# Kernel tuning notes

Hardware: AMD Instinct MI355X
Metric: run time of the kernel (lower is better)

Reference implementation:

```python
import jax, jax.numpy as jnp
from jax import lax
import numpy as np

K = 3          # sampling grid size (kernel_size)
WS = 4         # scope kernel size (weight_shape)
DILATION = 1


def setup_inputs() -> dict:
    key = jax.random.key(0)
    k1, k2, k3, k4 = jax.random.split(key, 4)
    x = jax.random.normal(k1, (4, 128, 56, 56), jnp.float32)
    # offset conv is zero-initialized in the original; use small values so offsets are realistic
    offset_w = jax.random.normal(k2, (2 * K * K, 128, K, K), jnp.float32) * 0.01
    offset_b = jax.random.normal(k3, (2 * K * K,), jnp.float32) * 0.01
    weight = jax.random.normal(k4, (128, WS, WS), jnp.float32) * 0.1  # depthwise scope kernel
    return {"x": x, "offset_w": offset_w, "offset_b": offset_b, "weight": weight}


def reference(x, offset_w, offset_b, weight):
    B, C, H, W = x.shape
    K2 = K * K
    # offset conv: 3x3, stride 1, pad 1 (same geometry as main conv)
    off = lax.conv_general_dilated(
        x, offset_w, window_strides=(1, 1), padding=[(1, 1), (1, 1)],
        dimension_numbers=("NCHW", "OIHW", "NCHW"))
    off = off + offset_b[None, :, None, None]
    off = off * DILATION                     # offset_clip is None
    off = off.reshape(B, K2, 2, H, W)
    dy, dx = off[:, :, 0], off[:, :, 1]      # [B,K2,H,W]

    # base coordinates of the KxK sampling grid centered inside the WSxWS scope kernel
    base = jnp.arange(K, dtype=x.dtype) - (K - 1) / 2 + (WS - 1) / 2   # [K]
    by = jnp.repeat(base, K)                 # k = i*K + j -> row i
    bx = jnp.tile(base, K)                   # k = i*K + j -> col j
    yc = dy + by[None, :, None, None]        # [B,K2,H,W] sampling coords in kernel space
    xc = dx + bx[None, :, None, None]

    # bilinear sampling of the scope kernel (zero outside scope)
    wflat = weight.reshape(C, WS * WS)
    y0 = jnp.floor(yc)
    x0 = jnp.floor(xc)
    samp = jnp.zeros((C, B, K2, H, W), x.dtype)
    for oy, ox in ((0, 0), (0, 1), (1, 0), (1, 1)):
        yi = y0 + oy
        xi = x0 + ox
        coef = (1.0 - jnp.abs(yc - yi)) * (1.0 - jnp.abs(xc - xi))
        valid = (yi >= 0) & (yi < WS) & (xi >= 0) & (xi < WS)
        idx = (jnp.clip(yi, 0, WS - 1) * WS + jnp.clip(xi, 0, WS - 1)).astype(jnp.int32)
        vals = jnp.take(wflat, idx, axis=1)  # [C,B,K2,H,W] irregular gather
        samp = samp + (coef * valid)[None] * vals
    samp = jnp.moveaxis(samp, 0, 1)          # [B,C,K2,H,W]

    # depthwise conv with per-pixel sampled kernels (stride 1, pad 1, dilation 1)
    xp = jnp.pad(x, ((0, 0), (0, 0), (1, 1), (1, 1)))
    pats = jnp.stack([xp[:, :, i:i + H, j:j + W] for i in range(K) for j in range(K)], axis=2)
    return jnp.sum(samp * pats, axis=2)      # [B,C,H,W]
```

## Files before the change

kernel.cpp:

```cpp
#include <hip/hip_runtime.h>

#define BB 4
#define CC 128
#define HH 56
#define WW 56
#define NK2 9
#define NO 18
#define WSZ 4
#define CG 8
#define CPG 16
#define W64 64

#define WSA_FLOATS (224L * CG * NO * W64)
#define WSC_ENTRIES (4L * NK2 * HH * W64)

__global__ __launch_bounds__(256) void conv_partial(
    const float* __restrict__ x,
    const float* __restrict__ offset_w,
    float* __restrict__ wsA)
{
    const int blk = blockIdx.x;
    const int bh  = blk >> 3;
    const int cg  = blk & 7;
    const int b   = bh / HH;
    const int h   = bh - b * HH;
    const int t   = threadIdx.x;
    const int lane = t & 63;
    const int wv  = __builtin_amdgcn_readfirstlane(t >> 6);

    __shared__ float s_red[4][NO][W64];

    float acc[NO];
    #pragma unroll
    for (int o = 0; o < NO; ++o) acc[o] = 0.f;

    const int c0 = cg * CPG + wv * 4;
    if (lane < WW) {
        const float* xb = x + (long)b * CC * HH * WW;
        #pragma unroll
        for (int ci = 0; ci < 4; ++ci) {
            const int c = c0 + ci;
            const float* xc = xb + c * HH * WW;
            #pragma unroll
            for (int ky = 0; ky < 3; ++ky) {
                const int hy = h + ky - 1;
                float x0 = 0.f, x1 = 0.f, x2 = 0.f;
                if (hy >= 0 && hy < HH) {
                    const float* r = xc + hy * WW;
                    x1 = r[lane];
                    x0 = (lane > 0)      ? r[lane - 1] : 0.f;
                    x2 = (lane < WW - 1) ? r[lane + 1] : 0.f;
                }
                const float* wp = offset_w + c * 9 + ky * 3;
                #pragma unroll
                for (int o = 0; o < NO; ++o) {
                    const float* wo = wp + o * (CC * 9);
                    acc[o] += x0 * wo[0] + x1 * wo[1] + x2 * wo[2];
                }
            }
        }
    }
    #pragma unroll
    for (int o = 0; o < NO; ++o) s_red[wv][o][lane] = acc[o];
    __syncthreads();

    const float* sr = (const float*)s_red;
    float* dst = wsA + (long)blk * (NO * W64);
    for (int s = t; s < NO * W64; s += 256) {
        dst[s] = sr[s] + sr[NO * W64 + s] + sr[2 * NO * W64 + s] + sr[3 * NO * W64 + s];
    }
}

__global__ __launch_bounds__(64) void coef_kernel(
    const float* __restrict__ wsA,
    const float* __restrict__ offset_b,
    float4* __restrict__ wsC,
    unsigned* __restrict__ wsI)
{
    const int blk = blockIdx.x;
    const int k2  = blk % NK2;
    const int bh  = blk / NK2;
    const int b   = bh / HH;
    const int h   = bh - b * HH;
    const int w   = threadIdx.x;

    const float* base = wsA + (long)bh * (CG * NO * W64);
    float dy = offset_b[2 * k2];
    float dx = offset_b[2 * k2 + 1];
    #pragma unroll
    for (int g = 0; g < CG; ++g) {
        dy += base[g * (NO * W64) + (2 * k2) * W64 + w];
        dx += base[g * (NO * W64) + (2 * k2 + 1) * W64 + w];
    }

    const float yc = dy + 0.5f + (float)(k2 / 3);
    const float xc = dx + 0.5f + (float)(k2 % 3);
    const float y0 = floorf(yc), x0f = floorf(xc);
    const float fy = yc - y0, fx = xc - x0f;
    const int yi = (int)y0, xi = (int)x0f;
    float cf[4]; int id[4];
    #pragma unroll
    for (int q = 0; q < 4; ++q) {
        const int oy = q >> 1, ox = q & 1;
        const int yy = yi + oy, xx = xi + ox;
        float c2 = (oy ? fy : 1.f - fy) * (ox ? fx : 1.f - fx);
        const bool valid = (yy >= 0) && (yy < WSZ) && (xx >= 0) && (xx < WSZ);
        cf[q] = valid ? c2 : 0.f;
        const int yyc = yy < 0 ? 0 : (yy > 3 ? 3 : yy);
        const int xxc = xx < 0 ? 0 : (xx > 3 ? 3 : xx);
        id[q] = yyc * 4 + xxc;
    }
    const long oidx = ((long)(b * NK2 + k2) * HH + h) * W64 + w;
    wsC[oidx] = make_float4(cf[0], cf[1], cf[2], cf[3]);
    wsI[oidx] = (unsigned)(id[0] | (id[1] << 4) | (id[2] << 8) | (id[3] << 12));
}

__global__ __launch_bounds__(256) void sample_kernel(
    const float* __restrict__ x,
    const float* __restrict__ weight,
    const float4* __restrict__ wsC,
    const unsigned* __restrict__ wsI,
    float* __restrict__ out)
{
    const int blk = blockIdx.x;
    const int bh  = blk >> 3;
    const int cg  = blk & 7;
    const int b   = bh / HH;
    const int h   = bh - b * HH;
    const int t   = threadIdx.x;
    const int lane = t & 63;
    const int wv  = __builtin_amdgcn_readfirstlane(t >> 6);

    __shared__ float s_w[CPG][16];
    if (t < CPG * 16) ((float*)s_w)[t] = weight[cg * CPG * 16 + t];
    __syncthreads();

    if (lane >= WW) return;
    const int w = lane;

    float4 cf[NK2]; unsigned pk[NK2];
    const long cidx0 = ((long)b * NK2 * HH + h) * W64 + w;
    #pragma unroll
    for (int k2 = 0; k2 < NK2; ++k2) {
        cf[k2] = wsC[cidx0 + (long)k2 * HH * W64];
        pk[k2] = wsI[cidx0 + (long)k2 * HH * W64];
    }

    const int cl0 = wv * 4;
    #pragma unroll
    for (int u = 0; u < 4; ++u) {
        const int cl = cl0 + u;
        const int c  = cg * CPG + cl;
        const float* xc = x + ((long)b * CC + c) * HH * WW;
        float xv[9];
        #pragma unroll
        for (int ky = 0; ky < 3; ++ky) {
            const int hy = h + ky - 1;
            #pragma unroll
            for (int kx = 0; kx < 3; ++kx) {
                const int wx = w + kx - 1;
                float v = 0.f;
                if (hy >= 0 && hy < HH && wx >= 0 && wx < WW)
                    v = xc[hy * WW + wx];
                xv[ky * 3 + kx] = v;
            }
        }
        float res = 0.f;
        #pragma unroll
        for (int k2 = 0; k2 < NK2; ++k2) {
            const unsigned p = pk[k2];
            const float samp = cf[k2].x * s_w[cl][p & 15]
                             + cf[k2].y * s_w[cl][(p >> 4) & 15]
                             + cf[k2].z * s_w[cl][(p >> 8) & 15]
                             + cf[k2].w * s_w[cl][(p >> 12) & 15];
            res += samp * xv[k2];
        }
        out[(((long)b * CC + c) * HH + h) * WW + w] = res;
    }
}

extern "C" void kernel_launch(void* const* d_in, const int* in_sizes, int n_in,
                              void* d_out, int out_size, void* d_ws, size_t ws_size,
                              hipStream_t stream) {
    const float* x        = (const float*)d_in[0];
    const float* offset_w = (const float*)d_in[1];
    const float* offset_b = (const float*)d_in[2];
    const float* weight   = (const float*)d_in[3];
    float* out = (float*)d_out;

    float*    wsA = (float*)d_ws;
    float4*   wsC = (float4*)((char*)d_ws + WSA_FLOATS * 4);
    unsigned* wsI = (unsigned*)((char*)d_ws + WSA_FLOATS * 4 + WSC_ENTRIES * 16);

    conv_partial <<<224 * CG, 256, 0, stream>>>(x, offset_w, wsA);
    coef_kernel  <<<224 * NK2, 64, 0, stream>>>(wsA, offset_b, wsC, wsI);
    sample_kernel<<<224 * CG, 256, 0, stream>>>(x, weight, wsC, wsI, out);
}
```

Measured before the change: 110.5 us.

## Compute two output rows per block in offset conv and stage weights in LDS

The offset-conv kernel now handles two output rows per block. It loads four input rows once and reuses each weight for both rows. Its weights are staged in shared memory and read as float4, replacing scattered global loads. The sampling kernel stores the scope weights transposed, so one float4 LDS read serves four channels at once. The cost is more registers and fewer blocks in the conv kernel, which may lower occupancy.

```diff
diff --git a/kernel.cpp b/kernel.cpp
--- a/kernel.cpp
+++ b/kernel.cpp
@@ -20,54 +20,85 @@
     float* __restrict__ wsA)
 {
     const int blk = blockIdx.x;
-    const int bh  = blk >> 3;
+    const int bh2 = blk >> 3;
     const int cg  = blk & 7;
-    const int b   = bh / HH;
-    const int h   = bh - b * HH;
+    const int b   = bh2 / 28;
+    const int h2  = bh2 - b * 28;
+    const int h0  = 2 * h2;
     const int t   = threadIdx.x;
     const int lane = t & 63;
     const int wv  = __builtin_amdgcn_readfirstlane(t >> 6);
 
-    __shared__ float s_red[4][NO][W64];
-
-    float acc[NO];
-    #pragma unroll
-    for (int o = 0; o < NO; ++o) acc[o] = 0.f;
-
-    const int c0 = cg * CPG + wv * 4;
+    __shared__ float s_wt[CPG][3][56];
+    __shared__ float s_red[4][2][NO][W64];
+
+    for (int i = t; i < CPG * 3 * 54; i += 256) {
+        const int ci = i / 162;
+        int r = i - ci * 162;
+        const int ky = r / 54;
+        r -= ky * 54;
+        const int o = r / 3, kx = r - o * 3;
+        s_wt[ci][ky][r] = offset_w[(o * CC + cg * CPG + ci) * 9 + ky * 3 + kx];
+    }
+    __syncthreads();
+
+    float acc[2][NO];
+    #pragma unroll
+    for (int r = 0; r < 2; ++r)
+        #pragma unroll
+        for (int o = 0; o < NO; ++o) acc[r][o] = 0.f;
+
     if (lane < WW) {
         const float* xb = x + (long)b * CC * HH * WW;
         #pragma unroll
         for (int ci = 0; ci < 4; ++ci) {
-            const int c = c0 + ci;
+            const int cl = wv * 4 + ci;
+            const int c  = cg * CPG + cl;
             const float* xc = xb + c * HH * WW;
+            float xr[4][3];
+            #pragma unroll
+            for (int r = 0; r < 4; ++r) {
+                const int hy = h0 + r - 1;
+                float v0 = 0.f, v1 = 0.f, v2 = 0.f;
+                if (hy >= 0 && hy < HH) {
+                    const float* row = xc + hy * WW;
+                    v1 = row[lane];
+                    v0 = (lane > 0)      ? row[lane - 1] : 0.f;
+                    v2 = (lane < WW - 1) ? row[lane + 1] : 0.f;
+                }
+                xr[r][0] = v0; xr[r][1] = v1; xr[r][2] = v2;
+            }
             #pragma unroll
             for (int ky = 0; ky < 3; ++ky) {
-                const int hy = h + ky - 1;
-                float x0 = 0.f, x1 = 0.f, x2 = 0.f;
-                if (hy >= 0 && hy < HH) {
-                    const float* r = xc + hy * WW;
-                    x1 = r[lane];
-                    x0 = (lane > 0)      ? r[lane - 1] : 0.f;
-                    x2 = (lane < WW - 1) ? r[lane + 1] : 0.f;
-                }
-                const float* wp = offset_w + c * 9 + ky * 3;
+                const float4* wq = (const float4*)&s_wt[cl][ky][0];
+                float4 w4[14];
                 #pragma unroll
-                for (int o = 0; o < NO; ++o) {
-                    const float* wo = wp + o * (CC * 9);
-                    acc[o] += x0 * wo[0] + x1 * wo[1] + x2 * wo[2];
+                for (int q = 0; q < 14; ++q) w4[q] = wq[q];
+                #pragma unroll
+                for (int f = 0; f < 54; ++f) {
+                    const int o = f / 3, kx = f - o * 3;
+                    const int q = f >> 2, e = f & 3;
+                    const float wv_ = (e == 0) ? w4[q].x : (e == 1) ? w4[q].y
+                                     : (e == 2) ? w4[q].z : w4[q].w;
+                    acc[0][o] += wv_ * xr[ky][kx];
+                    acc[1][o] += wv_ * xr[ky + 1][kx];
                 }
             }
         }
     }
     #pragma unroll
-    for (int o = 0; o < NO; ++o) s_red[wv][o][lane] = acc[o];
+    for (int r = 0; r < 2; ++r)
+        #pragma unroll
+        for (int o = 0; o < NO; ++o) s_red[wv][r][o][lane] = acc[r][o];
     __syncthreads();
 
     const float* sr = (const float*)s_red;
-    float* dst = wsA + (long)blk * (NO * W64);
-    for (int s = t; s < NO * W64; s += 256) {
-        dst[s] = sr[s] + sr[NO * W64 + s] + sr[2 * NO * W64 + s] + sr[3 * NO * W64 + s];
+    for (int s = t; s < 2 * NO * W64; s += 256) {
+        const float v = sr[s] + sr[2304 + s] + sr[2 * 2304 + s] + sr[3 * 2304 + s];
+        const int r = s / (NO * W64);
+        const int rem = s - r * (NO * W64);
+        const int bh = b * HH + h0 + r;
+        wsA[((long)bh * CG + cg) * (NO * W64) + rem] = v;
     }
 }
 
@@ -131,12 +162,16 @@
     const int lane = t & 63;
     const int wv  = __builtin_amdgcn_readfirstlane(t >> 6);
 
-    __shared__ float s_w[CPG][16];
-    if (t < CPG * 16) ((float*)s_w)[t] = weight[cg * CPG * 16 + t];
+    __shared__ float s_wT[16][20];
+    if (t < 256) {
+        const int j = t >> 4, cl = t & 15;
+        s_wT[j][cl] = weight[(cg * CPG + cl) * 16 + j];
+    }
     __syncthreads();
 
     if (lane >= WW) return;
     const int w = lane;
+    const int cl0 = wv * 4;
 
     float4 cf[NK2]; unsigned pk[NK2];
     const long cidx0 = ((long)b * NK2 * HH + h) * W64 + w;
@@ -146,13 +181,11 @@
         pk[k2] = wsI[cidx0 + (long)k2 * HH * W64];
     }
 
-    const int cl0 = wv * 4;
+    float xv[4][9];
     #pragma unroll
     for (int u = 0; u < 4; ++u) {
-        const int cl = cl0 + u;
-        const int c  = cg * CPG + cl;
+        const int c = cg * CPG + cl0 + u;
         const float* xc = x + ((long)b * CC + c) * HH * WW;
-        float xv[9];
         #pragma unroll
         for (int ky = 0; ky < 3; ++ky) {
             const int hy = h + ky - 1;
@@ -162,20 +195,33 @@
                 float v = 0.f;
                 if (hy >= 0 && hy < HH && wx >= 0 && wx < WW)
                     v = xc[hy * WW + wx];
-                xv[ky * 3 + kx] = v;
+                xv[u][ky * 3 + kx] = v;
             }
         }
-        float res = 0.f;
-        #pragma unroll
-        for (int k2 = 0; k2 < NK2; ++k2) {
-            const unsigned p = pk[k2];
-            const float samp = cf[k2].x * s_w[cl][p & 15]
-                             + cf[k2].y * s_w[cl][(p >> 4) & 15]
-                             + cf[k2].z * s_w[cl][(p >> 8) & 15]
-                             + cf[k2].w * s_w[cl][(p >> 12) & 15];
-            res += samp * xv[k2];
-        }
-        out[(((long)b * CC + c) * HH + h) * WW + w] = res;
+    }
+
+    float res[4] = {0.f, 0.f, 0.f, 0.f};
+    #pragma unroll
+    for (int k2 = 0; k2 < NK2; ++k2) {
+        const unsigned p = pk[k2];
+        const float4 W0 = *(const float4*)&s_wT[p & 15][cl0];
+        const float4 W1 = *(const float4*)&s_wT[(p >> 4) & 15][cl0];
+        const float4 W2 = *(const float4*)&s_wT[(p >> 8) & 15][cl0];
+        const float4 W3 = *(const float4*)&s_wT[(p >> 12) & 15][cl0];
+        const float4 c4 = cf[k2];
+        float samp[4];
+        samp[0] = c4.x * W0.x + c4.y * W1.x + c4.z * W2.x + c4.w * W3.x;
+        samp[1] = c4.x * W0.y + c4.y * W1.y + c4.z * W2.y + c4.w * W3.y;
+        samp[2] = c4.x * W0.z + c4.y * W1.z + c4.z * W2.z + c4.w * W3.z;
+        samp[3] = c4.x * W0.w + c4.y * W1.w + c4.z * W2.w + c4.w * W3.w;
+        #pragma unroll
+        for (int u = 0; u < 4; ++u) res[u] += samp[u] * xv[u][k2];
+    }
+
+    #pragma unroll
+    for (int u = 0; u < 4; ++u) {
+        const int c = cg * CPG + cl0 + u;
+        out[(((long)b * CC + c) * HH + h) * WW + w] = res[u];
     }
 }
 
@@ -192,7 +238,7 @@
     float4*   wsC = (float4*)((char*)d_ws + WSA_FLOATS * 4);
     unsigned* wsI = (unsigned*)((char*)d_ws + WSA_FLOATS * 4 + WSC_ENTRIES * 16);
 
-    conv_partial <<<224 * CG, 256, 0, stream>>>(x, offset_w, wsA);
+    conv_partial <<<BB * 28 * CG, 256, 0, stream>>>(x, offset_w, wsA);
     coef_kernel  <<<224 * NK2, 64, 0, stream>>>(wsA, offset_b, wsC, wsI);
     sample_kernel<<<224 * CG, 256, 0, stream>>>(x, weight, wsC, wsI, out);
 }
```

After: 125.0 us. 13.1% more time.
